# Optimization experiments

Hardware: AMD Instinct MI355X
Metric: run time of the kernel (lower is better)

The kernel has to match this reference:

```python
import jax, jax.numpy as jnp
import numpy as np

VOCAB = 30000; PAD = 0; H = 128; ROOT = 128; MAX_NODES = 1024; NUM_REL = 64
NL = MAX_NODES // ROOT - 1   # 7 leaves per root node (num_leaves)
LH = 4                       # head span length (all head_lengths == LH)
B = 64


def setup_inputs():
    key = jax.random.key(0)
    ks = jax.random.split(key, 6)
    # tokens >= 1 so no pad tokens: every leaf is populated -> all tail spans have length NL
    input_nodes = jax.random.randint(ks[0], (B, MAX_NODES, 1), 1, VOCAB, dtype=jnp.int32)
    leaf_relationships = jax.random.randint(ks[1], (B, ROOT), 1, NUM_REL + 1, dtype=jnp.int32)
    head_lengths = jnp.full((B, ROOT), LH, dtype=jnp.int32)
    atom_emb = (jax.random.normal(ks[2], (VOCAB, H), jnp.float32) * 0.02).at[PAD].set(0.0)
    rel_mat_emb = (jax.random.normal(ks[3], (NUM_REL + 1, H * H), jnp.float32) * 0.05).at[0].set(0.0)
    rel_emb = (jax.random.normal(ks[4], (NUM_REL + 1, 2 * H), jnp.float32) * 0.05).at[0].set(0.0)
    graph_token = jax.random.normal(ks[5], (1, H), jnp.float32) * 0.02
    return {"input_nodes": input_nodes, "leaf_relationships": leaf_relationships,
            "head_lengths": head_lengths, "atom_emb": atom_emb,
            "rel_mat_emb": rel_mat_emb, "rel_emb": rel_emb, "graph_token": graph_token}


def reference(input_nodes, leaf_relationships, head_lengths, atom_emb, rel_mat_emb, rel_emb, graph_token):
    Bq, N, F = input_nodes.shape          # F == 1 (required by original code's squeeze(1))
    node_feature = atom_emb[input_nodes].sum(axis=-2)   # [B,N,H], sum over atom-feature dim
    tok = input_nodes[..., 0]                           # [B,N]

    # head spans: one span per root node, start = root index, length LH, clamped like torch
    r_idx = jnp.arange(ROOT)
    head_pos = jnp.clip(r_idx[:, None] + jnp.arange(LH)[None, :], 0, ROOT - 1)   # [ROOT,LH]
    # tail spans: contiguous leaves per root, fixed length NL
    tail_pos = ROOT + r_idx[:, None] * NL + jnp.arange(NL)[None, :]              # [ROOT,NL]
    head_tok = tok[:, head_pos].reshape(Bq * ROOT, LH)
    tail_tok = tok[:, tail_pos].reshape(Bq * ROOT, NL)

    # triples ordered row-major over (batch, root) exactly like torch.nonzero
    rels = leaf_relationships.reshape(-1)                # [S], S = B*ROOT
    M = rel_mat_emb[rels].reshape(-1, H, H)              # [S,H,H] relation matrices (dropout is eval/identity)
    r = rel_emb[rels]                                    # [S,2H]
    he = atom_emb[head_tok]                              # [S,LH,H]
    te = atom_emb[tail_tok]                              # [S,NL,H]

    Mt = jnp.einsum('sij,stj->sti', M, te)               # M @ tail_embed per tail
    Mh = jnp.einsum('sij,shj->shi', M, he)               # M @ head_embed per head
    # torch views bmm output [H,2] as [2H] -> interleaved (Mt, Mh); r dotted with it:
    a = jnp.einsum('si,sti->st', r[:, 0::2], Mt)
    b = jnp.einsum('si,shi->sh', r[:, 1::2], Mh)
    scores = jax.nn.leaky_relu(a[:, :, None] + b[:, None, :], negative_slope=0.01)  # [S,NL,LH]
    alpha = jax.nn.softmax(scores, axis=-1)              # softmax over heads (dim=0 of [LH] in torch)
    hsum = jnp.einsum('sth,shj->stj', alpha, he)         # head_embed @ alphas
    final = jnp.einsum('sij,stj->sti', M, hsum)          # [S,NL,H]

    # scatter-add: destination node for triple (b,r), tail t is ROOT + r*NL + t -> contiguous leaf block
    node_feature = node_feature.at[:, ROOT:].add(final.reshape(Bq, ROOT * NL, H))
    gt = jnp.broadcast_to(graph_token[None], (Bq, 1, H))
    return jnp.concatenate([gt, node_feature], axis=1)   # [B, N+1, H]
```

## Files before the change

### kernel.cpp

```cpp
#include <hip/hip_runtime.h>
#include <hip/hip_bf16.h>
#include <stdint.h>

typedef unsigned int u32;

#define BATCH 64
#define ROOT 128
#define NLEAF 7
#define LHEAD 4
#define HDIM 128
#define NNODES 1024
#define OUTROWS 1025
#define NREL1 65

typedef __attribute__((ext_vector_type(8))) short bf16x8;
typedef __attribute__((ext_vector_type(4))) float f32x4;

__device__ float g_U[NREL1 * HDIM];
__device__ float g_V[NREL1 * HDIM];
__device__ u32   g_Mfrag[NREL1 * 8192];

static __device__ __forceinline__ u32 rne_bf16(float f) {
    u32 u = __builtin_bit_cast(u32, f);
    return (u + 0x7fffu + ((u >> 16) & 1u)) >> 16;
}
static __device__ __forceinline__ u32 pack_bf16(float a, float b) {
    return rne_bf16(a) | (rne_bf16(b) << 16);
}

__global__ void prep_kernel(const float* __restrict__ rel_mat,
                            const float* __restrict__ rel_emb) {
    int rel = blockIdx.x;
    int part = blockIdx.y;
    const float* M = rel_mat + (size_t)rel * HDIM * HDIM;
    __shared__ float red_u[8][32], red_v[8][32];

    if (part < 4) {
        u32* dst = &g_Mfrag[(size_t)rel * 8192];
        #pragma unroll
        for (int q = 0; q < 8; ++q) {
            int o = part * 2048 + q * 256 + threadIdx.x;
            int r  = o >> 10;
            int t  = (o >> 8) & 3;
            int ln = (o >> 2) & 63;
            int dw = o & 3;
            int i = r * 16 + (ln & 15);
            int j = t * 32 + ((ln >> 4) << 3) + dw * 2;
            dst[o] = pack_bf16(M[i * HDIM + j], M[i * HDIM + j + 1]);
        }
    } else {
        int p = part - 4;
        int jj = threadIdx.x & 31, s = threadIdx.x >> 5;
        int j = p * 32 + jj;
        const float* r = rel_emb + (size_t)rel * 2 * HDIM;
        float u = 0.f, v = 0.f;
        #pragma unroll
        for (int ii = 0; ii < 16; ++ii) {
            int i = s * 16 + ii;
            float m = M[i * HDIM + j];
            u += r[2 * i] * m;
            v += r[2 * i + 1] * m;
        }
        red_u[s][jj] = u; red_v[s][jj] = v;
        __syncthreads();
        if (s == 0) {
            float su = 0.f, sv = 0.f;
            #pragma unroll
            for (int q = 0; q < 8; ++q) { su += red_u[q][jj]; sv += red_v[q][jj]; }
            g_U[rel * HDIM + j] = su;
            g_V[rel * HDIM + j] = sv;
        }
    }
}

__global__ __launch_bounds__(256) void triple_kernel(
    const int* __restrict__ tok,
    const int* __restrict__ leaf_rel,
    const float* __restrict__ atom,
    const float* __restrict__ gtok,
    float* __restrict__ out)
{
    int g = blockIdx.x;
    int b = blockIdx.y;
    int tid = threadIdx.x;
    int wave = tid >> 6, lane = tid & 63;
    int rn = g * 4 + wave;

    __shared__ __align__(16) float MhT[4][LHEAD][HDIM];
    __shared__ float asb[4][16];
    __shared__ __align__(16) float alpha_s[4][NLEAF][LHEAD];
    __shared__ int stok[4][12];

    int rel = leaf_rel[b * ROOT + rn];

    if (lane < LHEAD + NLEAF) {
        int idx;
        if (lane < LHEAD) {
            int hp = rn + lane; if (hp > ROOT - 1) hp = ROOT - 1;
            idx = tok[b * NNODES + hp];
        } else {
            idx = tok[b * NNODES + ROOT + rn * NLEAF + (lane - LHEAD)];
        }
        stok[wave][lane] = idx;
    }

    const float* U = &g_U[rel * HDIM];
    const float* V = &g_V[rel * HDIM];
    float u_lo = U[lane], u_hi = U[lane + 64];
    float v_lo = V[lane], v_hi = V[lane + 64];

    #pragma unroll
    for (int d = 0; d < NLEAF + LHEAD; ++d) {
        int trow = (d < NLEAF) ? (LHEAD + d) : (d - NLEAF);
        const float* row = atom + (size_t)stok[wave][trow] * HDIM;
        float w0 = (d < NLEAF) ? u_lo : v_lo;
        float w1 = (d < NLEAF) ? u_hi : v_hi;
        float p = w0 * row[lane] + w1 * row[lane + 64];
        #pragma unroll
        for (int m = 32; m > 0; m >>= 1) p += __shfl_xor(p, m, 64);
        if (lane == 0) asb[wave][(d < NLEAF) ? d : (8 + d - NLEAF)] = p;
    }

    if (lane < NLEAF) {
        float av = asb[wave][lane];
        float sc[LHEAD];
        float mx = -1e30f;
        #pragma unroll
        for (int l = 0; l < LHEAD; ++l) {
            float x = av + asb[wave][8 + l];
            x = (x >= 0.f) ? x : 0.01f * x;
            sc[l] = x; mx = fmaxf(mx, x);
        }
        float sum = 0.f;
        #pragma unroll
        for (int l = 0; l < LHEAD; ++l) { sc[l] = __expf(sc[l] - mx); sum += sc[l]; }
        float inv = 1.f / sum;
        #pragma unroll
        for (int l = 0; l < LHEAD; ++l) alpha_s[wave][lane][l] = sc[l] * inv;
    }

    int nn = lane & 15;
    int kb = (lane >> 4) << 3;
    const float* hrow = atom + (size_t)stok[wave][nn & 3] * HDIM;
    uint4 bfr[4];
    #pragma unroll
    for (int t = 0; t < 4; ++t) {
        float4 f0 = *(const float4*)(hrow + t * 32 + kb);
        float4 f1 = *(const float4*)(hrow + t * 32 + kb + 4);
        bfr[t].x = pack_bf16(f0.x, f0.y);
        bfr[t].y = pack_bf16(f0.z, f0.w);
        bfr[t].z = pack_bf16(f1.x, f1.y);
        bfr[t].w = pack_bf16(f1.z, f1.w);
    }

    const uint4* Mf = ((const uint4*)g_Mfrag) + (size_t)rel * 2048;
    #pragma unroll
    for (int rt = 0; rt < 8; ++rt) {
        f32x4 acc = {0.f, 0.f, 0.f, 0.f};
        #pragma unroll
        for (int kt = 0; kt < 4; ++kt) {
            uint4 afr = Mf[(rt * 4 + kt) * 64 + lane];
            acc = __builtin_amdgcn_mfma_f32_16x16x32_bf16(
                      __builtin_bit_cast(bf16x8, afr),
                      __builtin_bit_cast(bf16x8, bfr[kt]), acc, 0, 0, 0);
        }
        if (nn < LHEAD) {
            int row0 = rt * 16 + ((lane >> 4) << 2);
            *(float4*)&MhT[wave][nn][row0] =
                make_float4(acc[0], acc[1], acc[2], acc[3]);
        }
    }

    size_t bbase = (size_t)b * OUTROWS * HDIM;
    {
        const float* rrow = atom + (size_t)stok[wave][0] * HDIM;
        out[bbase + (size_t)(1 + rn) * HDIM + lane]      = rrow[lane];
        out[bbase + (size_t)(1 + rn) * HDIM + lane + 64] = rrow[lane + 64];
        if (g == 0 && wave == 0) {
            out[bbase + lane]      = gtok[lane];
            out[bbase + lane + 64] = gtok[lane + 64];
        }
    }

    size_t obase = bbase + (size_t)(1 + ROOT + rn * NLEAF) * HDIM;
    #pragma unroll
    for (int e = 0; e < 14; ++e) {
        int idx = e * 64 + lane;
        int t = idx >> 7, j = idx & 127;
        float tev = atom[(size_t)stok[wave][LHEAD + t] * HDIM + j];
        float4 al = *(const float4*)&alpha_s[wave][t][0];
        float r = tev + al.x * MhT[wave][0][j] + al.y * MhT[wave][1][j]
                      + al.z * MhT[wave][2][j] + al.w * MhT[wave][3][j];
        out[obase + idx] = r;
    }
}

extern "C" void kernel_launch(void* const* d_in, const int* in_sizes, int n_in,
                              void* d_out, int out_size, void* d_ws, size_t ws_size,
                              hipStream_t stream) {
    (void)in_sizes; (void)n_in; (void)out_size; (void)d_ws; (void)ws_size;
    const int* tok       = (const int*)d_in[0];
    const int* leaf_rel  = (const int*)d_in[1];
    const float* atom    = (const float*)d_in[3];
    const float* rel_mat = (const float*)d_in[4];
    const float* rel_emb = (const float*)d_in[5];
    const float* gtok    = (const float*)d_in[6];
    float* out = (float*)d_out;

    dim3 pgrid(NREL1, 8);
    prep_kernel<<<pgrid, 256, 0, stream>>>(rel_mat, rel_emb);

    dim3 grid(ROOT / 4, BATCH);
    triple_kernel<<<grid, 256, 0, stream>>>(tok, leaf_rel, atom, gtok, out);
}
```

Before: 117.4 us.

## Keep gathered embeddings in registers and compute softmax redundantly per lane

Each wave now loads its head and tail embedding rows once into registers, broadcasting token indices with shuffles instead of staging them in shared memory. Those register copies feed the attention dot products, the bf16 MFMA operand (through a padded shared head buffer), the root copy and the final residual add, so the repeated global gathers of the same rows go away. Softmax is computed redundantly in every lane from register-held scores, which drops the shared scratch arrays and the lane-restricted phase. The cost is more registers per thread and duplicated exp work.

```diff
diff --git a/kernel.cpp b/kernel.cpp
--- a/kernel.cpp
+++ b/kernel.cpp
@@ -12,6 +12,7 @@
 #define NNODES 1024
 #define OUTROWS 1025
 #define NREL1 65
+#define PSTR 132
 
 typedef __attribute__((ext_vector_type(8))) short bf16x8;
 typedef __attribute__((ext_vector_type(4))) float f32x4;
@@ -86,22 +87,34 @@
     int wave = tid >> 6, lane = tid & 63;
     int rn = g * 4 + wave;
 
-    __shared__ __align__(16) float MhT[4][LHEAD][HDIM];
-    __shared__ float asb[4][16];
-    __shared__ __align__(16) float alpha_s[4][NLEAF][LHEAD];
-    __shared__ int stok[4][12];
+    __shared__ __align__(16) float he_s[4][LHEAD][PSTR];
+    __shared__ __align__(16) float MhT[4][LHEAD][PSTR];
 
     int rel = leaf_rel[b * ROOT + rn];
 
+    int tokidx = 0;
     if (lane < LHEAD + NLEAF) {
-        int idx;
-        if (lane < LHEAD) {
-            int hp = rn + lane; if (hp > ROOT - 1) hp = ROOT - 1;
-            idx = tok[b * NNODES + hp];
-        } else {
-            idx = tok[b * NNODES + ROOT + rn * NLEAF + (lane - LHEAD)];
-        }
-        stok[wave][lane] = idx;
+        int pos;
+        if (lane < LHEAD) { int hp = rn + lane; if (hp > ROOT - 1) hp = ROOT - 1; pos = hp; }
+        else              pos = ROOT + rn * NLEAF + (lane - LHEAD);
+        tokidx = tok[b * NNODES + pos];
+    }
+    int htok[LHEAD], ttok[NLEAF];
+    #pragma unroll
+    for (int l = 0; l < LHEAD; ++l) htok[l] = __shfl(tokidx, l, 64);
+    #pragma unroll
+    for (int t = 0; t < NLEAF; ++t) ttok[t] = __shfl(tokidx, LHEAD + t, 64);
+
+    float he_lo[LHEAD], he_hi[LHEAD], te_lo[NLEAF], te_hi[NLEAF];
+    #pragma unroll
+    for (int l = 0; l < LHEAD; ++l) {
+        const float* r = atom + (size_t)htok[l] * HDIM;
+        he_lo[l] = r[lane]; he_hi[l] = r[lane + 64];
+    }
+    #pragma unroll
+    for (int t = 0; t < NLEAF; ++t) {
+        const float* r = atom + (size_t)ttok[t] * HDIM;
+        te_lo[t] = r[lane]; te_hi[t] = r[lane + 64];
     }
 
     const float* U = &g_U[rel * HDIM];
@@ -110,43 +123,35 @@
     float v_lo = V[lane], v_hi = V[lane + 64];
 
     #pragma unroll
-    for (int d = 0; d < NLEAF + LHEAD; ++d) {
-        int trow = (d < NLEAF) ? (LHEAD + d) : (d - NLEAF);
-        const float* row = atom + (size_t)stok[wave][trow] * HDIM;
-        float w0 = (d < NLEAF) ? u_lo : v_lo;
-        float w1 = (d < NLEAF) ? u_hi : v_hi;
-        float p = w0 * row[lane] + w1 * row[lane + 64];
+    for (int l = 0; l < LHEAD; ++l) {
+        he_s[wave][l][lane]      = he_lo[l];
+        he_s[wave][l][lane + 64] = he_hi[l];
+    }
+
+    float a_r[NLEAF], b_r[LHEAD];
+    #pragma unroll
+    for (int t = 0; t < NLEAF; ++t) {
+        float p = u_lo * te_lo[t] + u_hi * te_hi[t];
         #pragma unroll
         for (int m = 32; m > 0; m >>= 1) p += __shfl_xor(p, m, 64);
-        if (lane == 0) asb[wave][(d < NLEAF) ? d : (8 + d - NLEAF)] = p;
-    }
-
-    if (lane < NLEAF) {
-        float av = asb[wave][lane];
-        float sc[LHEAD];
-        float mx = -1e30f;
-        #pragma unroll
-        for (int l = 0; l < LHEAD; ++l) {
-            float x = av + asb[wave][8 + l];
-            x = (x >= 0.f) ? x : 0.01f * x;
-            sc[l] = x; mx = fmaxf(mx, x);
-        }
-        float sum = 0.f;
-        #pragma unroll
-        for (int l = 0; l < LHEAD; ++l) { sc[l] = __expf(sc[l] - mx); sum += sc[l]; }
-        float inv = 1.f / sum;
-        #pragma unroll
-        for (int l = 0; l < LHEAD; ++l) alpha_s[wave][lane][l] = sc[l] * inv;
+        a_r[t] = p;
+    }
+    #pragma unroll
+    for (int l = 0; l < LHEAD; ++l) {
+        float p = v_lo * he_lo[l] + v_hi * he_hi[l];
+        #pragma unroll
+        for (int m = 32; m > 0; m >>= 1) p += __shfl_xor(p, m, 64);
+        b_r[l] = p;
     }
 
     int nn = lane & 15;
     int kb = (lane >> 4) << 3;
-    const float* hrow = atom + (size_t)stok[wave][nn & 3] * HDIM;
     uint4 bfr[4];
     #pragma unroll
     for (int t = 0; t < 4; ++t) {
-        float4 f0 = *(const float4*)(hrow + t * 32 + kb);
-        float4 f1 = *(const float4*)(hrow + t * 32 + kb + 4);
+        const float* h = &he_s[wave][nn & 3][t * 32 + kb];
+        float4 f0 = *(const float4*)h;
+        float4 f1 = *(const float4*)(h + 4);
         bfr[t].x = pack_bf16(f0.x, f0.y);
         bfr[t].y = pack_bf16(f0.z, f0.w);
         bfr[t].z = pack_bf16(f1.x, f1.y);
@@ -166,32 +171,41 @@
         }
         if (nn < LHEAD) {
             int row0 = rt * 16 + ((lane >> 4) << 2);
-            *(float4*)&MhT[wave][nn][row0] =
-                make_float4(acc[0], acc[1], acc[2], acc[3]);
+            *(float4*)&MhT[wave][nn][row0] = make_float4(acc[0], acc[1], acc[2], acc[3]);
         }
     }
 
     size_t bbase = (size_t)b * OUTROWS * HDIM;
-    {
-        const float* rrow = atom + (size_t)stok[wave][0] * HDIM;
-        out[bbase + (size_t)(1 + rn) * HDIM + lane]      = rrow[lane];
-        out[bbase + (size_t)(1 + rn) * HDIM + lane + 64] = rrow[lane + 64];
-        if (g == 0 && wave == 0) {
-            out[bbase + lane]      = gtok[lane];
-            out[bbase + lane + 64] = gtok[lane + 64];
-        }
+    out[bbase + (size_t)(1 + rn) * HDIM + lane]      = he_lo[0];
+    out[bbase + (size_t)(1 + rn) * HDIM + lane + 64] = he_hi[0];
+    if (g == 0 && wave == 0) {
+        out[bbase + lane]      = gtok[lane];
+        out[bbase + lane + 64] = gtok[lane + 64];
     }
 
     size_t obase = bbase + (size_t)(1 + ROOT + rn * NLEAF) * HDIM;
     #pragma unroll
-    for (int e = 0; e < 14; ++e) {
-        int idx = e * 64 + lane;
-        int t = idx >> 7, j = idx & 127;
-        float tev = atom[(size_t)stok[wave][LHEAD + t] * HDIM + j];
-        float4 al = *(const float4*)&alpha_s[wave][t][0];
-        float r = tev + al.x * MhT[wave][0][j] + al.y * MhT[wave][1][j]
-                      + al.z * MhT[wave][2][j] + al.w * MhT[wave][3][j];
-        out[obase + idx] = r;
+    for (int t = 0; t < NLEAF; ++t) {
+        float sc[LHEAD]; float mx = -1e30f;
+        #pragma unroll
+        for (int l = 0; l < LHEAD; ++l) {
+            float x = a_r[t] + b_r[l];
+            x = (x >= 0.f) ? x : 0.01f * x;
+            sc[l] = x; mx = fmaxf(mx, x);
+        }
+        float sum = 0.f;
+        #pragma unroll
+        for (int l = 0; l < LHEAD; ++l) { sc[l] = __expf(sc[l] - mx); sum += sc[l]; }
+        float inv = 1.f / sum;
+        float r0 = te_lo[t], r1 = te_hi[t];
+        #pragma unroll
+        for (int l = 0; l < LHEAD; ++l) {
+            float al = sc[l] * inv;
+            r0 += al * MhT[wave][l][lane];
+            r1 += al * MhT[wave][l][lane + 64];
+        }
+        out[obase + t * HDIM + lane]      = r0;
+        out[obase + t * HDIM + lane + 64] = r1;
     }
 }
 
```

New measurement: 110.6 us, median of 2. -5.8%, faster.
